# Performance work log

Hardware: AMD Instinct MI355X
Metric: run time of the kernel (lower is better)

Reference implementation:

```python
import jax, jax.numpy as jnp
import numpy as np

# Dims: B nodes, Z species (elements), IN/OUT channels, M = 2*l+1 (l=1)
B, Z, IN, OUT, M = 8192, 10, 512, 512, 3
ALPHA = 1.0 / np.sqrt(IN)  # self.alpha = 1/sqrt(in_dim)
SQRT3 = float(np.sqrt(3.0))


def setup_inputs() -> dict:
    key = jax.random.key(0)
    k1, k2, k3 = jax.random.split(key, 3)
    t = jax.random.normal(k1, (B, IN, M), dtype=jnp.float32)
    species = jax.random.randint(k2, (B,), 0, Z)
    node_attrs = jax.nn.one_hot(species, Z, dtype=jnp.float32)  # [B, Z] one-hot
    # torch.nn.init.uniform_(weights, -sqrt(3), sqrt(3))
    weights = jax.random.uniform(k3, (Z, OUT, IN), dtype=jnp.float32,
                                 minval=-SQRT3, maxval=SQRT3)
    return {"t": t, "node_attrs": node_attrs, "weights": weights}


def reference(t, node_attrs, weights):
    # Faithful to: einsum('bz, zCc, bcd -> bCd', node_attrs, weights*alpha, t)
    # Contract weights with t first per species ([Z,B,C,M], ~500MB), which
    # avoids the huge [B,C,c] per-node weight-gather intermediate, then
    # select/sum over species with the one-hot node_attrs.
    W = weights * ALPHA                       # [Z, OUT, IN]
    zt = jnp.einsum('zCc,bcd->zbCd', W, t)    # [Z, B, OUT, M]
    out = jnp.einsum('bz,zbCd->bCd', node_attrs, zt)  # [B, OUT, M]
    return out
```

## Files before the change

kernel.cpp:

```cpp
#include <hip/hip_runtime.h>
#include <stdint.h>

#define NB   8192
#define NZ   10
#define CIN  512
#define COUT 512
#define MM   3
#define ALPHA 0.04419417382415922f

#define ROWS_TOTAL (NB * MM)
#define BM 128
#define BN 64
#define BK 32
#define KITERS (CIN / BK)
#define MAX_MT (ROWS_TOTAL / BM + NZ)
#define NGRP 32

typedef short bf16x8 __attribute__((ext_vector_type(8)));
typedef float f32x4  __attribute__((ext_vector_type(4)));

__device__ __forceinline__ uint16_t f2bf(float f) {
    union { float f; uint32_t i; } v; v.f = f;
    uint32_t x = v.i;
    x += 0x7fffu + ((x >> 16) & 1u);
    return (uint16_t)(x >> 16);
}
__device__ __forceinline__ uint32_t pack2(float a, float b) {
    return (uint32_t)f2bf(a) | ((uint32_t)f2bf(b) << 16);
}
__device__ __forceinline__ void async16(const ushort* g, ushort* l) {
    __builtin_amdgcn_global_load_lds((const uint32_t*)g, (uint32_t*)l, 16, 0, 0);
}

__global__ __launch_bounds__(256)
void prep_kernel(const float* __restrict__ attrs, const float* __restrict__ w,
                 int* __restrict__ species, int* __restrict__ hist,
                 ushort* __restrict__ wt) {
    const int tid = threadIdx.x;
    if (blockIdx.x >= NGRP) {
        const size_t i = ((size_t)(blockIdx.x - NGRP) * 256 + tid) * 8;
        float4 a = *(const float4*)(w + i);
        float4 b = *(const float4*)(w + i + 4);
        uint4 o;
        o.x = pack2(a.x, a.y); o.y = pack2(a.z, a.w);
        o.z = pack2(b.x, b.y); o.w = pack2(b.z, b.w);
        *(uint4*)(wt + i) = o;
        return;
    }
    __shared__ int wc[4][NZ];
    const int b = blockIdx.x * 256 + tid;
    const float* a = attrs + (size_t)b * NZ;
    int s = 0;
    #pragma unroll
    for (int z = 0; z < NZ; z++) if (a[z] > 0.5f) s = z;
    species[b] = s;
    const int wv = tid >> 6, lane = tid & 63;
    #pragma unroll
    for (int z = 0; z < NZ; z++) {
        unsigned long long m = __ballot(s == z);
        if (lane == 0) wc[wv][z] = __popcll(m);
    }
    __syncthreads();
    if (tid < NZ) {
        hist[blockIdx.x * NZ + tid] = wc[0][tid] + wc[1][tid] + wc[2][tid] + wc[3][tid];
    }
}

__global__ __launch_bounds__(256)
void place_kernel(const int* __restrict__ species, const int* __restrict__ hist,
                  int* __restrict__ sorted, int* __restrict__ offsets,
                  int* __restrict__ tile_offsets) {
    __shared__ int lhist[NGRP][NZ];
    __shared__ int loff[NZ + 1], ltoff[NZ + 1];
    __shared__ int pb[NZ];
    __shared__ int wc[4][NZ];
    const int tid = threadIdx.x, g = blockIdx.x;

    for (int i = tid; i < NGRP * NZ; i += 256) ((int*)lhist)[i] = hist[i];
    __syncthreads();
    if (tid == 0) {
        int off = 0, toff = 0;
        for (int z = 0; z < NZ; z++) {
            int tot = 0;
            for (int gg = 0; gg < NGRP; gg++) tot += lhist[gg][z];
            loff[z] = off; ltoff[z] = toff;
            off += tot;
            toff += (3 * tot + BM - 1) / BM;
        }
        loff[NZ] = off; ltoff[NZ] = toff;
    }
    __syncthreads();
    if (tid < NZ) {
        int base = loff[tid];
        for (int gg = 0; gg < g; gg++) base += lhist[gg][tid];
        pb[tid] = base;
    }
    if (g == 0 && tid < NZ + 1) {
        offsets[tid] = loff[tid];
        tile_offsets[tid] = ltoff[tid];
    }
    const int b = g * 256 + tid;
    const int s = species[b];
    const int wv = tid >> 6, lane = tid & 63;
    unsigned long long mymask = 0;
    #pragma unroll
    for (int z = 0; z < NZ; z++) {
        unsigned long long m = __ballot(s == z);
        if (lane == 0) wc[wv][z] = __popcll(m);
        if (s == z) mymask = m;
    }
    __syncthreads();
    int rank = __popcll(mymask & ((1ull << lane) - 1ull));
    #pragma unroll
    for (int w2 = 0; w2 < 4; w2++) if (w2 < wv) rank += wc[w2][s];
    sorted[pb[s] + rank] = b;
}

__global__ __launch_bounds__(256)
void pack_t(const float* __restrict__ t, const int* __restrict__ sorted,
            ushort* __restrict__ tt) {
    const int w = threadIdx.x >> 6, L = threadIdx.x & 63;
    const int p = blockIdx.x * 4 + w;
    const int node = sorted[p];
    const float4* src = (const float4*)(t + (size_t)node * (CIN * MM) + L * 24);
    float4 f[6];
    #pragma unroll
    for (int i = 0; i < 6; i++) f[i] = src[i];
    const float* v = (const float*)f;
    #pragma unroll
    for (int d = 0; d < MM; d++) {
        uint4 o;
        o.x = pack2(v[d],      v[3 + d]);
        o.y = pack2(v[6 + d],  v[9 + d]);
        o.z = pack2(v[12 + d], v[15 + d]);
        o.w = pack2(v[18 + d], v[21 + d]);
        *(uint4*)&tt[(size_t)(3 * p + d) * CIN + L * 8] = o;
    }
}

__global__ __launch_bounds__(256)
void gemm_kernel(const ushort* __restrict__ tt, const ushort* __restrict__ wt,
                 const int* __restrict__ sorted, const int* __restrict__ offsets,
                 const int* __restrict__ tile_offsets, float* __restrict__ out) {
    __shared__ ushort As[BM][BK];
    __shared__ ushort Bs[BN][BK];
    __shared__ int spos[48];

    const int tz = blockIdx.x;
    if (tz >= tile_offsets[NZ]) return;
    int z = 0;
    #pragma unroll
    for (int i = 1; i < NZ; i++) if (tile_offsets[i] <= tz) z = i;

    const int row_base = 3 * offsets[z] + (tz - tile_offsets[z]) * BM;
    const int row_end  = 3 * offsets[z + 1];
    const int pos0     = row_base / 3;
    const int Cbase    = blockIdx.y * BN;

    const int tid = threadIdx.x;
    const int w = tid >> 6, L = tid & 63;

    if (tid < 48) spos[tid] = sorted[min(pos0 + tid, NB - 1)];

    const int lrow = L >> 2;
    const int lk   = (L & 3) * 8;
    const ushort* gA = tt + (size_t)(row_base + w * 32 + lrow) * CIN + lk;
    const ushort* gB = wt + ((size_t)z * COUT + Cbase + w * 16 + lrow) * CIN + lk;
    ushort* lA0 = &As[w * 32][0];
    ushort* lA1 = &As[w * 32 + 16][0];
    ushort* lB0 = &Bs[w * 16][0];

    const int wm = w & 1, wn = w >> 1;
    const int q = L >> 4, mr = L & 15;

    f32x4 acc[4][2];
    #pragma unroll
    for (int i = 0; i < 4; i++)
        #pragma unroll
        for (int j = 0; j < 2; j++) acc[i][j] = (f32x4){0.f, 0.f, 0.f, 0.f};

    for (int kt = 0; kt < KITERS; kt++) {
        const int ko = kt * BK;
        async16(gA + ko, lA0);
        async16(gA + (size_t)16 * CIN + ko, lA1);
        async16(gB + ko, lB0);
        __syncthreads();

        bf16x8 af[4], bf[2];
        #pragma unroll
        for (int am = 0; am < 4; am++)
            af[am] = *(const bf16x8*)&As[wm * 64 + am * 16 + mr][q * 8];
        #pragma unroll
        for (int bn = 0; bn < 2; bn++)
            bf[bn] = *(const bf16x8*)&Bs[wn * 32 + bn * 16 + mr][q * 8];
        #pragma unroll
        for (int am = 0; am < 4; am++)
            #pragma unroll
            for (int bn = 0; bn < 2; bn++)
                acc[am][bn] = __builtin_amdgcn_mfma_f32_16x16x32_bf16(
                    af[am], bf[bn], acc[am][bn], 0, 0, 0);
        __syncthreads();
    }

    #pragma unroll
    for (int am = 0; am < 4; am++) {
        #pragma unroll
        for (int r = 0; r < 4; r++) {
            const int Rg = row_base + wm * 64 + am * 16 + q * 4 + r;
            if (Rg < row_end) {
                const int pos = Rg / 3;
                const int d = Rg - 3 * pos;
                const int node = spos[pos - pos0];
                float* o = out + (size_t)node * (COUT * MM) + d;
                #pragma unroll
                for (int bn = 0; bn < 2; bn++) {
                    const int Cg = Cbase + wn * 32 + bn * 16 + mr;
                    o[(size_t)Cg * 3] = ALPHA * acc[am][bn][r];
                }
            }
        }
    }
}

extern "C" void kernel_launch(void* const* d_in, const int* in_sizes, int n_in,
                              void* d_out, int out_size, void* d_ws, size_t ws_size,
                              hipStream_t stream) {
    const float* t     = (const float*)d_in[0];
    const float* attrs = (const float*)d_in[1];
    const float* w     = (const float*)d_in[2];
    float* out = (float*)d_out;

    uint8_t* ws = (uint8_t*)d_ws;
    int* species      = (int*)ws;                  ws += NB * 4;
    int* sorted       = (int*)ws;                  ws += NB * 4;
    int* hist         = (int*)ws;                  ws += NGRP * NZ * 4;
    int* offsets      = (int*)ws;                  ws += 16 * 4;
    int* tile_offsets = (int*)ws;                  ws += 16 * 4;
    ws = (uint8_t*)(((uintptr_t)ws + 255) & ~(uintptr_t)255);
    ushort* wt = (ushort*)ws;                      ws += (size_t)NZ * COUT * CIN * 2;
    ushort* tt = (ushort*)ws;

    hipLaunchKernelGGL(prep_kernel, dim3(NGRP + (NZ * COUT * CIN) / 2048), dim3(256),
                       0, stream, attrs, w, species, hist, wt);
    hipLaunchKernelGGL(place_kernel, dim3(NGRP), dim3(256), 0, stream,
                       species, hist, sorted, offsets, tile_offsets);
    hipLaunchKernelGGL(pack_t, dim3(NB / 4), dim3(256), 0, stream, t, sorted, tt);
    hipLaunchKernelGGL(gemm_kernel, dim3(MAX_MT, COUT / BN), dim3(256), 0, stream,
                       tt, wt, sorted, offsets, tile_offsets, out);
}
```

Baseline: 159.7 us.

## Fold t conversion into prep kernel, gather rows in GEMM, widen N tile

The bf16 conversion of t moves into the prep kernel and keeps original node order, so the separate pack_t launch, which needed the sort result, is removed. The GEMM now gathers A rows through the sorted index per row instead of reading a pre-sorted buffer. BN doubles to 128, giving each wave a 4x4 MFMA accumulator block and halving the grid's N dimension. Loads and stores use nontemporal hints. The trade-offs are scattered A-row loads, more registers per thread, and fewer blocks in flight.

Result: slower. 222.4 us (+39.3%).

```diff
diff --git a/kernel.cpp b/kernel.cpp
--- a/kernel.cpp
+++ b/kernel.cpp
@@ -10,14 +10,17 @@
 
 #define ROWS_TOTAL (NB * MM)
 #define BM 128
-#define BN 64
+#define BN 128
 #define BK 32
 #define KITERS (CIN / BK)
 #define MAX_MT (ROWS_TOTAL / BM + NZ)
 #define NGRP 32
+#define PW_BLOCKS 320
+#define PT_BLOCKS 2048
 
 typedef short bf16x8 __attribute__((ext_vector_type(8)));
 typedef float f32x4  __attribute__((ext_vector_type(4)));
+typedef uint32_t u32x4 __attribute__((ext_vector_type(4)));
 
 __device__ __forceinline__ uint16_t f2bf(float f) {
     union { float f; uint32_t i; } v; v.f = f;
@@ -33,36 +36,58 @@
 }
 
 __global__ __launch_bounds__(256)
-void prep_kernel(const float* __restrict__ attrs, const float* __restrict__ w,
-                 int* __restrict__ species, int* __restrict__ hist,
-                 ushort* __restrict__ wt) {
+void prep_kernel(const float* __restrict__ t, const float* __restrict__ attrs,
+                 const float* __restrict__ w, int* __restrict__ species,
+                 int* __restrict__ hist, ushort* __restrict__ wt,
+                 ushort* __restrict__ tb) {
     const int tid = threadIdx.x;
-    if (blockIdx.x >= NGRP) {
-        const size_t i = ((size_t)(blockIdx.x - NGRP) * 256 + tid) * 8;
-        float4 a = *(const float4*)(w + i);
-        float4 b = *(const float4*)(w + i + 4);
-        uint4 o;
-        o.x = pack2(a.x, a.y); o.y = pack2(a.z, a.w);
-        o.z = pack2(b.x, b.y); o.w = pack2(b.z, b.w);
-        *(uint4*)(wt + i) = o;
-        return;
-    }
-    __shared__ int wc[4][NZ];
-    const int b = blockIdx.x * 256 + tid;
-    const float* a = attrs + (size_t)b * NZ;
-    int s = 0;
-    #pragma unroll
-    for (int z = 0; z < NZ; z++) if (a[z] > 0.5f) s = z;
-    species[b] = s;
     const int wv = tid >> 6, lane = tid & 63;
-    #pragma unroll
-    for (int z = 0; z < NZ; z++) {
-        unsigned long long m = __ballot(s == z);
-        if (lane == 0) wc[wv][z] = __popcll(m);
-    }
-    __syncthreads();
-    if (tid < NZ) {
-        hist[blockIdx.x * NZ + tid] = wc[0][tid] + wc[1][tid] + wc[2][tid] + wc[3][tid];
+
+    if (blockIdx.x < NGRP) {
+        __shared__ int wc[4][NZ];
+        const int b = blockIdx.x * 256 + tid;
+        const float* a = attrs + (size_t)b * NZ;
+        int s = 0;
+        #pragma unroll
+        for (int z = 0; z < NZ; z++) if (a[z] > 0.5f) s = z;
+        species[b] = s;
+        #pragma unroll
+        for (int z = 0; z < NZ; z++) {
+            unsigned long long m = __ballot(s == z);
+            if (lane == 0) wc[wv][z] = __popcll(m);
+        }
+        __syncthreads();
+        if (tid < NZ)
+            hist[blockIdx.x * NZ + tid] = wc[0][tid] + wc[1][tid] + wc[2][tid] + wc[3][tid];
+    } else if (blockIdx.x < NGRP + PW_BLOCKS) {
+        const size_t base = (size_t)(blockIdx.x - NGRP) * 8192;
+        #pragma unroll
+        for (int e = 0; e < 4; e++) {
+            const size_t i = base + ((size_t)e * 256 + tid) * 8;
+            f32x4 a = __builtin_nontemporal_load((const f32x4*)(w + i));
+            f32x4 b = __builtin_nontemporal_load((const f32x4*)(w + i) + 1);
+            u32x4 o;
+            o.x = pack2(a.x, a.y); o.y = pack2(a.z, a.w);
+            o.z = pack2(b.x, b.y); o.w = pack2(b.z, b.w);
+            __builtin_nontemporal_store(o, (u32x4*)(wt + i));
+        }
+    } else {
+        const int p = (blockIdx.x - NGRP - PW_BLOCKS) * 4 + wv;
+        const f32x4* src = (const f32x4*)(t + (size_t)p * (CIN * MM) + lane * 24);
+        f32x4 f[6];
+        #pragma unroll
+        for (int i = 0; i < 6; i++) f[i] = __builtin_nontemporal_load(src + i);
+        const float* v = (const float*)f;
+        #pragma unroll
+        for (int d = 0; d < MM; d++) {
+            u32x4 o;
+            o.x = pack2(v[d],      v[3 + d]);
+            o.y = pack2(v[6 + d],  v[9 + d]);
+            o.z = pack2(v[12 + d], v[15 + d]);
+            o.w = pack2(v[18 + d], v[21 + d]);
+            __builtin_nontemporal_store(
+                o, (u32x4*)&tb[(size_t)(3 * p + d) * CIN + lane * 8]);
+        }
     }
 }
 
@@ -117,86 +142,72 @@
 }
 
 __global__ __launch_bounds__(256)
-void pack_t(const float* __restrict__ t, const int* __restrict__ sorted,
-            ushort* __restrict__ tt) {
-    const int w = threadIdx.x >> 6, L = threadIdx.x & 63;
-    const int p = blockIdx.x * 4 + w;
-    const int node = sorted[p];
-    const float4* src = (const float4*)(t + (size_t)node * (CIN * MM) + L * 24);
-    float4 f[6];
-    #pragma unroll
-    for (int i = 0; i < 6; i++) f[i] = src[i];
-    const float* v = (const float*)f;
-    #pragma unroll
-    for (int d = 0; d < MM; d++) {
-        uint4 o;
-        o.x = pack2(v[d],      v[3 + d]);
-        o.y = pack2(v[6 + d],  v[9 + d]);
-        o.z = pack2(v[12 + d], v[15 + d]);
-        o.w = pack2(v[18 + d], v[21 + d]);
-        *(uint4*)&tt[(size_t)(3 * p + d) * CIN + L * 8] = o;
-    }
-}
-
-__global__ __launch_bounds__(256)
-void gemm_kernel(const ushort* __restrict__ tt, const ushort* __restrict__ wt,
+void gemm_kernel(const ushort* __restrict__ tb, const ushort* __restrict__ wt,
                  const int* __restrict__ sorted, const int* __restrict__ offsets,
                  const int* __restrict__ tile_offsets, float* __restrict__ out) {
     __shared__ ushort As[BM][BK];
     __shared__ ushort Bs[BN][BK];
     __shared__ int spos[48];
 
-    const int tz = blockIdx.x;
-    if (tz >= tile_offsets[NZ]) return;
+    const int mt = blockIdx.x;
+    if (mt >= tile_offsets[NZ]) return;
     int z = 0;
     #pragma unroll
-    for (int i = 1; i < NZ; i++) if (tile_offsets[i] <= tz) z = i;
-
-    const int row_base = 3 * offsets[z] + (tz - tile_offsets[z]) * BM;
+    for (int i = 1; i < NZ; i++) if (tile_offsets[i] <= mt) z = i;
+
+    const int row_base = 3 * offsets[z] + (mt - tile_offsets[z]) * BM;
     const int row_end  = 3 * offsets[z + 1];
     const int pos0     = row_base / 3;
     const int Cbase    = blockIdx.y * BN;
 
     const int tid = threadIdx.x;
-    const int w = tid >> 6, L = tid & 63;
+    const int wv = tid >> 6, lane = tid & 63;
 
     if (tid < 48) spos[tid] = sorted[min(pos0 + tid, NB - 1)];
 
-    const int lrow = L >> 2;
-    const int lk   = (L & 3) * 8;
-    const ushort* gA = tt + (size_t)(row_base + w * 32 + lrow) * CIN + lk;
-    const ushort* gB = wt + ((size_t)z * COUT + Cbase + w * 16 + lrow) * CIN + lk;
-    ushort* lA0 = &As[w * 32][0];
-    ushort* lA1 = &As[w * 32 + 16][0];
-    ushort* lB0 = &Bs[w * 16][0];
-
-    const int wm = w & 1, wn = w >> 1;
-    const int q = L >> 4, mr = L & 15;
-
-    f32x4 acc[4][2];
+    const int lrow = lane >> 2;
+    const int lk   = (lane & 3) * 8;
+    const int r0 = min(row_base + wv * 32 + lrow,      row_end - 1);
+    const int r1 = min(row_base + wv * 32 + 16 + lrow, row_end - 1);
+    const int p0 = r0 / 3, d0 = r0 - 3 * p0;
+    const int p1 = r1 / 3, d1 = r1 - 3 * p1;
+    const ushort* gA0 = tb + ((size_t)sorted[p0] * 3 + d0) * CIN + lk;
+    const ushort* gA1 = tb + ((size_t)sorted[p1] * 3 + d1) * CIN + lk;
+    const ushort* gB0 = wt + ((size_t)z * COUT + Cbase + wv * 32 + lrow) * CIN + lk;
+    const ushort* gB1 = gB0 + (size_t)16 * CIN;
+    ushort* lA0 = &As[wv * 32][0];
+    ushort* lA1 = &As[wv * 32 + 16][0];
+    ushort* lB0 = &Bs[wv * 32][0];
+    ushort* lB1 = &Bs[wv * 32 + 16][0];
+
+    const int wm = wv & 1, wn = wv >> 1;
+    const int q = lane >> 4, mr = lane & 15;
+
+    f32x4 acc[4][4];
     #pragma unroll
     for (int i = 0; i < 4; i++)
         #pragma unroll
-        for (int j = 0; j < 2; j++) acc[i][j] = (f32x4){0.f, 0.f, 0.f, 0.f};
+        for (int j = 0; j < 4; j++) acc[i][j] = (f32x4){0.f, 0.f, 0.f, 0.f};
 
     for (int kt = 0; kt < KITERS; kt++) {
         const int ko = kt * BK;
-        async16(gA + ko, lA0);
-        async16(gA + (size_t)16 * CIN + ko, lA1);
-        async16(gB + ko, lB0);
+        async16(gA0 + ko, lA0);
+        async16(gA1 + ko, lA1);
+        async16(gB0 + ko, lB0);
+        async16(gB1 + ko, lB1);
         __syncthreads();
 
-        bf16x8 af[4], bf[2];
+        bf16x8 af[4], bf[4];
         #pragma unroll
         for (int am = 0; am < 4; am++)
             af[am] = *(const bf16x8*)&As[wm * 64 + am * 16 + mr][q * 8];
         #pragma unroll
-        for (int bn = 0; bn < 2; bn++)
-            bf[bn] = *(const bf16x8*)&Bs[wn * 32 + bn * 16 + mr][q * 8];
+        for (int bn = 0; bn < 4; bn++)
+            bf[bn] = *(const bf16x8*)&Bs[wn * 64 + bn * 16 + mr][q * 8];
         #pragma unroll
         for (int am = 0; am < 4; am++)
             #pragma unroll
-            for (int bn = 0; bn < 2; bn++)
+            for (int bn = 0; bn < 4; bn++)
                 acc[am][bn] = __builtin_amdgcn_mfma_f32_16x16x32_bf16(
                     af[am], bf[bn], acc[am][bn], 0, 0, 0);
         __syncthreads();
@@ -213,9 +224,10 @@
                 const int node = spos[pos - pos0];
                 float* o = out + (size_t)node * (COUT * MM) + d;
                 #pragma unroll
-                for (int bn = 0; bn < 2; bn++) {
-                    const int Cg = Cbase + wn * 32 + bn * 16 + mr;
-                    o[(size_t)Cg * 3] = ALPHA * acc[am][bn][r];
+                for (int bn = 0; bn < 4; bn++) {
+                    const int Cg = Cbase + wn * 64 + bn * 16 + mr;
+                    __builtin_nontemporal_store(ALPHA * acc[am][bn][r],
+                                                o + (size_t)Cg * 3);
                 }
             }
         }
@@ -238,13 +250,12 @@
     int* tile_offsets = (int*)ws;                  ws += 16 * 4;
     ws = (uint8_t*)(((uintptr_t)ws + 255) & ~(uintptr_t)255);
     ushort* wt = (ushort*)ws;                      ws += (size_t)NZ * COUT * CIN * 2;
-    ushort* tt = (ushort*)ws;
-
-    hipLaunchKernelGGL(prep_kernel, dim3(NGRP + (NZ * COUT * CIN) / 2048), dim3(256),
-                       0, stream, attrs, w, species, hist, wt);
+    ushort* tb = (ushort*)ws;
+
+    hipLaunchKernelGGL(prep_kernel, dim3(NGRP + PW_BLOCKS + PT_BLOCKS), dim3(256),
+                       0, stream, t, attrs, w, species, hist, wt, tb);
     hipLaunchKernelGGL(place_kernel, dim3(NGRP), dim3(256), 0, stream,
                        species, hist, sorted, offsets, tile_offsets);
-    hipLaunchKernelGGL(pack_t, dim3(NB / 4), dim3(256), 0, stream, t, sorted, tt);
     hipLaunchKernelGGL(gemm_kernel, dim3(MAX_MT, COUT / BN), dim3(256), 0, stream,
-                       tt, wt, sorted, offsets, tile_offsets, out);
-}
+                       tb, wt, sorted, offsets, tile_offsets, out);
+}
```
